# Performance work log

Hardware: AMD Instinct MI355X
Metric: run time of the kernel (lower is better)

Reference implementation:

```python
import jax, jax.numpy as jnp
import numpy as np

B, N, C = 8, 1024, 768
H, D = 12, 64  # num_heads, head_dim
SCALE = D ** -0.5


def setup_inputs() -> dict:
    key = jax.random.key(0)
    ks = jax.random.split(key, 6)
    x = jax.random.normal(ks[0], (B, N, C), dtype=jnp.float32)
    # per-head Linear weights stacked: [H, D, C] (torch Linear stores [out, in])
    Wq = jax.random.normal(ks[1], (H, D, C), dtype=jnp.float32) * 0.02
    Wk = jax.random.normal(ks[2], (H, D, C), dtype=jnp.float32) * 0.02
    Wv = jax.random.normal(ks[3], (H, D, C), dtype=jnp.float32) * 0.02
    Wp = jax.random.normal(ks[4], (C, C), dtype=jnp.float32) * 0.02
    bp = jnp.zeros((C,), dtype=jnp.float32)
    return {"x": x, "Wq": Wq, "Wk": Wk, "Wv": Wv, "Wp": Wp, "bp": bp}


def reference(x, Wq, Wk, Wv, Wp, bp):
    # Per-head projections (batched across heads): [B, H, N, D]
    q = jnp.einsum('bnc,hdc->bhnd', x, Wq) * SCALE
    k = jnp.einsum('bnc,hdc->bhnd', x, Wk)
    v = jnp.einsum('bnc,hdc->bhnd', x, Wv)
    # Scaled dot-product attention per head
    attn = jax.nn.softmax(jnp.einsum('bhnd,bhmd->bhnm', q, k), axis=-1)
    out = jnp.einsum('bhnm,bhmd->bhnd', attn, v)
    # Concat heads along last dim == transpose to [B, N, H, D] then reshape
    out = out.transpose(0, 2, 1, 3).reshape(x.shape[0], x.shape[1], -1)
    # Output projection
    return out @ Wp.T + bp
```

## Files before the change

kernel.cpp:

```cpp
#include <hip/hip_runtime.h>

typedef unsigned short u16;
typedef __attribute__((ext_vector_type(8))) __bf16 bf16x8;
typedef __attribute__((ext_vector_type(4))) float f32x4;
typedef __attribute__((ext_vector_type(16))) float f32x16;

__device__ __forceinline__ u16 f2bf(float f) {
    union { float f; unsigned u; } v; v.f = f;
    unsigned u = v.u;
    u += 0x7FFFu + ((u >> 16) & 1u);
    return (u16)(u >> 16);
}

__device__ __forceinline__ unsigned pk2(float lo, float hi) {
    union { __bf16 h[2]; unsigned u; } x;
    x.h[0] = (__bf16)lo; x.h[1] = (__bf16)hi;
    return x.u;
}
__device__ __forceinline__ void pswap(unsigned &a, unsigned &b) {
    auto r = __builtin_amdgcn_permlane32_swap(a, b, false, false);
    a = r[0]; b = r[1];
}

typedef const __attribute__((address_space(1))) void GV;
typedef __attribute__((address_space(3))) void LV;
__device__ __forceinline__ void gl2lds16(const void* g, void* l) {
    __builtin_amdgcn_global_load_lds((GV*)g, (LV*)l, 16, 0, 0);
}

__global__ __launch_bounds__(256) void cast_all(
    const float* __restrict__ x,  const float* __restrict__ Wq,
    const float* __restrict__ Wk, const float* __restrict__ Wv,
    const float* __restrict__ Wp,
    u16* __restrict__ xb, u16* __restrict__ wb, u16* __restrict__ wpb)
{
    int bid = blockIdx.x;
    const float4* s; ushort4* d; int idx;
    if (bid < 6144) {
        s = (const float4*)x; d = (ushort4*)xb; idx = bid * 256 + threadIdx.x;
    } else {
        int t = bid - 6144;
        int w = t / 576;
        idx = (t - w * 576) * 256 + threadIdx.x;
        s = (const float4*)(w == 0 ? Wq : w == 1 ? Wk : w == 2 ? Wv : Wp);
        d = (ushort4*)(w == 3 ? wpb : wb + w * 589824);
    }
    float4 f = s[idx];
    ushort4 o;
    o.x = f2bf(f.x); o.y = f2bf(f.y); o.z = f2bf(f.z); o.w = f2bf(f.w);
    d[idx] = o;
}

__device__ __forceinline__ void stage_g(const u16* src, int k0, u16* lds, int g, int tid) {
    int i = g * 512 + tid;
    int row = i >> 3, p = i & 7;
    int l = p ^ (row & 7);
    gl2lds16(src + (size_t)row * 768 + k0 + l * 8, lds + i * 8);
}
__device__ __forceinline__ const bf16x8* frag64(const u16* lds, int row, int kc) {
    return reinterpret_cast<const bf16x8*>(lds + row * 64 + ((kc ^ (row & 7)) * 8));
}

__device__ __forceinline__ void kloop256(
    const u16* __restrict__ aSrc, const u16* __restrict__ bSrc,
    u16* As, u16* Bs, f32x4 (&acc)[4][4],
    int tid, int wm, int wn, int quad, int l16)
{
    #pragma unroll
    for (int tt = 0; tt < 2; tt++) {
        #pragma unroll
        for (int g = 0; g < 4; g++) stage_g(aSrc, tt * 64, As + tt * 16384, g, tid);
        #pragma unroll
        for (int g = 0; g < 2; g++) stage_g(bSrc, tt * 64, Bs + tt * 8192, g, tid);
    }
    asm volatile("s_waitcnt vmcnt(6)" ::: "memory");
    __builtin_amdgcn_s_barrier();
    asm volatile("" ::: "memory");

    int buf = 0;
    for (int t = 0; t < 12; t++) {
        const u16* Ab = As + buf * 16384;
        const u16* Bb = Bs + buf * 8192;
        int sb = buf + 2; if (sb >= 3) sb -= 3;
        u16* Asb = As + sb * 16384;
        u16* Bsb = Bs + sb * 8192;
        const bool pf = (t + 2 < 12);
        const int k2 = (t + 2) * 64;

        bf16x8 a[4], b[4];
        #pragma unroll
        for (int mi = 0; mi < 4; mi++) a[mi] = *frag64(Ab, wm * 64 + mi * 16 + l16, quad);
        #pragma unroll
        for (int ni = 0; ni < 4; ni++) b[ni] = *frag64(Bb, wn * 64 + ni * 16 + l16, quad);
        if (pf) {
            stage_g(aSrc, k2, Asb, 0, tid);
            stage_g(aSrc, k2, Asb, 1, tid);
            stage_g(aSrc, k2, Asb, 2, tid);
        }
        __builtin_amdgcn_s_barrier();
        asm volatile("" ::: "memory");
        __builtin_amdgcn_s_setprio(1);
        #pragma unroll
        for (int mi = 0; mi < 4; mi++)
            #pragma unroll
            for (int ni = 0; ni < 4; ni++)
                acc[mi][ni] = __builtin_amdgcn_mfma_f32_16x16x32_bf16(a[mi], b[ni], acc[mi][ni], 0, 0, 0);
        __builtin_amdgcn_s_setprio(0);

        #pragma unroll
        for (int mi = 0; mi < 4; mi++) a[mi] = *frag64(Ab, wm * 64 + mi * 16 + l16, 4 + quad);
        #pragma unroll
        for (int ni = 0; ni < 4; ni++) b[ni] = *frag64(Bb, wn * 64 + ni * 16 + l16, 4 + quad);
        if (pf) {
            stage_g(aSrc, k2, Asb, 3, tid);
            stage_g(bSrc, k2, Bsb, 0, tid);
            stage_g(bSrc, k2, Bsb, 1, tid);
        }
        if (t <= 9)       asm volatile("s_waitcnt vmcnt(6)" ::: "memory");
        else if (t == 10) asm volatile("s_waitcnt vmcnt(0)" ::: "memory");
        __builtin_amdgcn_s_barrier();
        asm volatile("" ::: "memory");
        __builtin_amdgcn_s_setprio(1);
        #pragma unroll
        for (int mi = 0; mi < 4; mi++)
            #pragma unroll
            for (int ni = 0; ni < 4; ni++)
                acc[mi][ni] = __builtin_amdgcn_mfma_f32_16x16x32_bf16(a[mi], b[ni], acc[mi][ni], 0, 0, 0);
        __builtin_amdgcn_s_setprio(0);

        buf++; if (buf == 3) buf = 0;
    }
}

__global__ __launch_bounds__(512, 2) void gemm_qkv(
    const u16* __restrict__ A, const u16* __restrict__ Bm,
    u16* __restrict__ qo, u16* __restrict__ ko, u16* __restrict__ vto)
{
    __shared__ u16 As[3][16384];
    __shared__ u16 Bs[3][8192];
    const int tid = threadIdx.x;
    const int wave = tid >> 6, lane = tid & 63;
    const int quad = lane >> 4, l16 = lane & 15;
    const int wm = wave >> 1, wn = wave & 1;
    const int id = blockIdx.x + 18 * blockIdx.y;
    const int nid = (id & 7) * 72 + (id >> 3);
    const int bx = nid % 18, by = nid / 18;
    const int rowBase = by * 256;
    const int colBase = bx * 128;

    f32x4 acc[4][4] = {};
    kloop256(A + (size_t)rowBase * 768, Bm + (size_t)colBase * 768,
             &As[0][0], &Bs[0][0], acc, tid, wm, wn, quad, l16);

    #pragma unroll
    for (int mi = 0; mi < 4; mi++) {
        #pragma unroll
        for (int ni = 0; ni < 4; ni++) {
            int gj = colBase + wn * 64 + ni * 16 + l16;
            int which = gj / 768;
            int r = gj - which * 768;
            int h = r >> 6, d = r & 63;
            int gi0 = rowBase + wm * 64 + mi * 16 + quad * 4;
            int b_ = gi0 >> 10;
            int n0 = gi0 & 1023;
            if (which == 2) {
                ushort4 pk;
                pk.x = f2bf(acc[mi][ni][0]);
                pk.y = f2bf(acc[mi][ni][1]);
                pk.z = f2bf(acc[mi][ni][2]);
                pk.w = f2bf(acc[mi][ni][3]);
                *reinterpret_cast<ushort4*>(vto + ((size_t)(b_ * 12 + h) * 64 + d) * 1024 + n0) = pk;
            } else {
                float s = (which == 0) ? 0.125f : 1.0f;
                u16* dst = (which == 0 ? qo : ko) + ((size_t)(b_ * 12 + h) * 1024 + n0) * 64 + d;
                #pragma unroll
                for (int rr = 0; rr < 4; rr++)
                    dst[(size_t)rr * 64] = f2bf(acc[mi][ni][rr] * s);
            }
        }
    }
}

__global__ __launch_bounds__(256, 3) void attn_fwd(
    const u16* __restrict__ q, const u16* __restrict__ k,
    const u16* __restrict__ vt, u16* __restrict__ ao)
{
    __shared__ u16 Ks[2][4096];
    __shared__ u16 Vs[2][4096];
    const int bh = blockIdx.x, qt = blockIdx.y;
    const int b = bh / 12, h = bh - b * 12;
    const int tid = threadIdx.x;
    const int wave = tid >> 6, lane = tid & 63;
    const int l31 = lane & 31, hi = lane >> 5;
    const int sw = l31 & 7;

    const u16* qb = q + (size_t)bh * 65536 + ((size_t)qt * 128 + wave * 32) * 64;
    const u16* kb = k + (size_t)bh * 65536;
    const u16* vb = vt + (size_t)bh * 65536;

    auto stage = [&](int buf, int j0) {
        #pragma unroll
        for (int r = 0; r < 2; r++) {
            int i = r * 256 + tid;
            int row = i >> 3, cp = i & 7;
            int cl = cp ^ (row & 7);
            gl2lds16((const char*)kb + (size_t)(j0 + row) * 128 + cl * 16,
                     (char*)&Ks[buf][0] + i * 16);
        }
        #pragma unroll
        for (int r = 0; r < 2; r++) {
            int i = r * 256 + tid;
            int row = i >> 3, cp = i & 7;
            int cl = cp ^ (row & 7);
            gl2lds16((const char*)vb + (size_t)row * 2048 + (size_t)j0 * 2 + cl * 16,
                     (char*)&Vs[buf][0] + i * 16);
        }
    };

    stage(0, 0);

    bf16x8 qf[4];
    #pragma unroll
    for (int dk = 0; dk < 4; dk++)
        qf[dk] = *reinterpret_cast<const bf16x8*>(qb + l31 * 64 + dk * 16 + hi * 8);

    f32x16 o0 = {}, o1 = {};
    float lsum = 0.f;

    __syncthreads();

    int buf = 0;
    for (int j0 = 0; j0 < 1024; j0 += 64) {
        if (j0 + 64 < 1024) stage(buf ^ 1, j0 + 64);

        f32x16 s0 = {}, s1 = {};
        #pragma unroll
        for (int dk = 0; dk < 4; dk++) {
            int ch = ((2 * dk + hi) ^ sw) * 8;
            bf16x8 kf0 = *reinterpret_cast<const bf16x8*>(&Ks[buf][l31 * 64 + ch]);
            bf16x8 kf1 = *reinterpret_cast<const bf16x8*>(&Ks[buf][(32 + l31) * 64 + ch]);
            s0 = __builtin_amdgcn_mfma_f32_32x32x16_bf16(kf0, qf[dk], s0, 0, 0, 0);
            s1 = __builtin_amdgcn_mfma_f32_32x32x16_bf16(kf1, qf[dk], s1, 0, 0, 0);
        }

        bf16x8 pa[4];
        #pragma unroll
        for (int kbk = 0; kbk < 2; kbk++) {
            float p[16];
            #pragma unroll
            for (int r = 0; r < 16; r++) {
                p[r] = __expf(kbk ? s1[r] : s0[r]);
                lsum += p[r];
            }
            unsigned W00 = pk2(p[0],  p[1]),  W01 = pk2(p[2],  p[3]);
            unsigned W10 = pk2(p[4],  p[5]),  W11 = pk2(p[6],  p[7]);
            unsigned W20 = pk2(p[8],  p[9]),  W21 = pk2(p[10], p[11]);
            unsigned W30 = pk2(p[12], p[13]), W31 = pk2(p[14], p[15]);
            pswap(W00, W10); pswap(W01, W11);
            pswap(W20, W30); pswap(W21, W31);
            union { unsigned u[4]; bf16x8 v; } pk0, pk1;
            pk0.u[0] = W00; pk0.u[1] = W01; pk0.u[2] = W10; pk0.u[3] = W11;
            pk1.u[0] = W20; pk1.u[1] = W21; pk1.u[2] = W30; pk1.u[3] = W31;
            pa[kbk * 2 + 0] = pk0.v;
            pa[kbk * 2 + 1] = pk1.v;
        }

        #pragma unroll
        for (int ks = 0; ks < 4; ks++) {
            int ch = ((2 * ks + hi) ^ sw) * 8;
            bf16x8 vf0 = *reinterpret_cast<const bf16x8*>(&Vs[buf][l31 * 64 + ch]);
            bf16x8 vf1 = *reinterpret_cast<const bf16x8*>(&Vs[buf][(32 + l31) * 64 + ch]);
            o0 = __builtin_amdgcn_mfma_f32_32x32x16_bf16(pa[ks], vf0, o0, 0, 0, 0);
            o1 = __builtin_amdgcn_mfma_f32_32x32x16_bf16(pa[ks], vf1, o1, 0, 0, 0);
        }

        __syncthreads();
        buf ^= 1;
    }

    lsum += __shfl_xor(lsum, 32, 64);

    #pragma unroll
    for (int r = 0; r < 16; r++) {
        int qrow = (r & 3) + 8 * (r >> 2) + 4 * hi;
        float lv = __shfl(lsum, qrow, 32);
        float inv = 1.0f / lv;
        int n = qt * 128 + wave * 32 + qrow;
        size_t base = (size_t)(b * 1024 + n) * 768 + h * 64;
        ao[base + l31]      = f2bf(o0[r] * inv);
        ao[base + 32 + l31] = f2bf(o1[r] * inv);
    }
}

__global__ __launch_bounds__(512, 2) void gemm_proj(
    const u16* __restrict__ A, const u16* __restrict__ Bm,
    const float* __restrict__ bias, float* __restrict__ out)
{
    __shared__ u16 As[3][16384];
    __shared__ u16 Bs[3][8192];
    const int tid = threadIdx.x;
    const int wave = tid >> 6, lane = tid & 63;
    const int quad = lane >> 4, l16 = lane & 15;
    const int wm = wave >> 1, wn = wave & 1;
    const int id = blockIdx.x + 6 * blockIdx.y;
    const int nid = (id & 7) * 24 + (id >> 3);
    const int bx = nid % 6, by = nid / 6;
    const int rowBase = by * 256;
    const int colBase = bx * 128;

    f32x4 acc[4][4] = {};
    kloop256(A + (size_t)rowBase * 768, Bm + (size_t)colBase * 768,
             &As[0][0], &Bs[0][0], acc, tid, wm, wn, quad, l16);

    #pragma unroll
    for (int mi = 0; mi < 4; mi++) {
        #pragma unroll
        for (int ni = 0; ni < 4; ni++) {
            int gj = colBase + wn * 64 + ni * 16 + l16;
            float bv = bias[gj];
            int gi0 = rowBase + wm * 64 + mi * 16 + quad * 4;
            #pragma unroll
            for (int rr2 = 0; rr2 < 4; rr2++)
                out[(size_t)(gi0 + rr2) * 768 + gj] = acc[mi][ni][rr2] + bv;
        }
    }
}

extern "C" void kernel_launch(void* const* d_in, const int* in_sizes, int n_in,
                              void* d_out, int out_size, void* d_ws, size_t ws_size,
                              hipStream_t stream) {
    const float* x  = (const float*)d_in[0];
    const float* Wq = (const float*)d_in[1];
    const float* Wk = (const float*)d_in[2];
    const float* Wv = (const float*)d_in[3];
    const float* Wp = (const float*)d_in[4];
    const float* bp = (const float*)d_in[5];
    float* out = (float*)d_out;

    u16* xb  = (u16*)d_ws;
    u16* wb  = xb  + 6291456;
    u16* wpb = wb  + 1769472;
    u16* qo  = wpb + 589824;
    u16* ko  = qo  + 6291456;
    u16* vto = ko  + 6291456;
    u16* ao  = vto + 6291456;

    cast_all<<<8448, 256, 0, stream>>>(x, Wq, Wk, Wv, Wp, xb, wb, wpb);
    gemm_qkv<<<dim3(18, 32), 512, 0, stream>>>(xb, wb, qo, ko, vto);
    attn_fwd<<<dim3(96, 8), 256, 0, stream>>>(qo, ko, vto, ao);
    gemm_proj<<<dim3(6, 32), 512, 0, stream>>>(ao, wpb, bp, out);
}
```

Measured before the change: 189.4 us.

## Halve GEMM K-step to 32 with new LDS layout and smaller proj tiles

Both GEMMs now step K by 32 instead of 64 and use a new swizzled LDS layout that packs two rows per 64-element line. This shrinks shared memory per block so more blocks fit per CU (the launch bounds ask for 4 blocks for qkv and 3 for proj). The projection GEMM is retiled to 128x128 blocks of 256 threads, which doubles its grid to raise occupancy and fill the GPU better. The cost is twice as many loop iterations and barriers, with less MFMA work between each synchronisation.

Measured after the change: 187.3 us. Within noise of the previous version (-1.1%).

```diff
diff --git a/kernel.cpp b/kernel.cpp
--- a/kernel.cpp
+++ b/kernel.cpp
@@ -51,93 +51,24 @@
     d[idx] = o;
 }
 
-__device__ __forceinline__ void stage_g(const u16* src, int k0, u16* lds, int g, int tid) {
-    int i = g * 512 + tid;
-    int row = i >> 3, p = i & 7;
-    int l = p ^ (row & 7);
-    gl2lds16(src + (size_t)row * 768 + k0 + l * 8, lds + i * 8);
-}
-__device__ __forceinline__ const bf16x8* frag64(const u16* lds, int row, int kc) {
-    return reinterpret_cast<const bf16x8*>(lds + row * 64 + ((kc ^ (row & 7)) * 8));
-}
-
-__device__ __forceinline__ void kloop256(
-    const u16* __restrict__ aSrc, const u16* __restrict__ bSrc,
-    u16* As, u16* Bs, f32x4 (&acc)[4][4],
-    int tid, int wm, int wn, int quad, int l16)
-{
-    #pragma unroll
-    for (int tt = 0; tt < 2; tt++) {
-        #pragma unroll
-        for (int g = 0; g < 4; g++) stage_g(aSrc, tt * 64, As + tt * 16384, g, tid);
-        #pragma unroll
-        for (int g = 0; g < 2; g++) stage_g(bSrc, tt * 64, Bs + tt * 8192, g, tid);
-    }
-    asm volatile("s_waitcnt vmcnt(6)" ::: "memory");
-    __builtin_amdgcn_s_barrier();
-    asm volatile("" ::: "memory");
-
-    int buf = 0;
-    for (int t = 0; t < 12; t++) {
-        const u16* Ab = As + buf * 16384;
-        const u16* Bb = Bs + buf * 8192;
-        int sb = buf + 2; if (sb >= 3) sb -= 3;
-        u16* Asb = As + sb * 16384;
-        u16* Bsb = Bs + sb * 8192;
-        const bool pf = (t + 2 < 12);
-        const int k2 = (t + 2) * 64;
-
-        bf16x8 a[4], b[4];
-        #pragma unroll
-        for (int mi = 0; mi < 4; mi++) a[mi] = *frag64(Ab, wm * 64 + mi * 16 + l16, quad);
-        #pragma unroll
-        for (int ni = 0; ni < 4; ni++) b[ni] = *frag64(Bb, wn * 64 + ni * 16 + l16, quad);
-        if (pf) {
-            stage_g(aSrc, k2, Asb, 0, tid);
-            stage_g(aSrc, k2, Asb, 1, tid);
-            stage_g(aSrc, k2, Asb, 2, tid);
-        }
-        __builtin_amdgcn_s_barrier();
-        asm volatile("" ::: "memory");
-        __builtin_amdgcn_s_setprio(1);
-        #pragma unroll
-        for (int mi = 0; mi < 4; mi++)
-            #pragma unroll
-            for (int ni = 0; ni < 4; ni++)
-                acc[mi][ni] = __builtin_amdgcn_mfma_f32_16x16x32_bf16(a[mi], b[ni], acc[mi][ni], 0, 0, 0);
-        __builtin_amdgcn_s_setprio(0);
-
-        #pragma unroll
-        for (int mi = 0; mi < 4; mi++) a[mi] = *frag64(Ab, wm * 64 + mi * 16 + l16, 4 + quad);
-        #pragma unroll
-        for (int ni = 0; ni < 4; ni++) b[ni] = *frag64(Bb, wn * 64 + ni * 16 + l16, 4 + quad);
-        if (pf) {
-            stage_g(aSrc, k2, Asb, 3, tid);
-            stage_g(bSrc, k2, Bsb, 0, tid);
-            stage_g(bSrc, k2, Bsb, 1, tid);
-        }
-        if (t <= 9)       asm volatile("s_waitcnt vmcnt(6)" ::: "memory");
-        else if (t == 10) asm volatile("s_waitcnt vmcnt(0)" ::: "memory");
-        __builtin_amdgcn_s_barrier();
-        asm volatile("" ::: "memory");
-        __builtin_amdgcn_s_setprio(1);
-        #pragma unroll
-        for (int mi = 0; mi < 4; mi++)
-            #pragma unroll
-            for (int ni = 0; ni < 4; ni++)
-                acc[mi][ni] = __builtin_amdgcn_mfma_f32_16x16x32_bf16(a[mi], b[ni], acc[mi][ni], 0, 0, 0);
-        __builtin_amdgcn_s_setprio(0);
-
-        buf++; if (buf == 3) buf = 0;
-    }
-}
-
-__global__ __launch_bounds__(512, 2) void gemm_qkv(
+__device__ __forceinline__ void stage_c(const u16* src, int k0, u16* lds, int i) {
+    int line = i >> 3, pos = i & 7;
+    int p = pos ^ (line & 7);
+    int r = line * 2 + (p >> 2), c = p & 3;
+    gl2lds16(src + (size_t)r * 768 + k0 + c * 8, lds + i * 8);
+}
+__device__ __forceinline__ const bf16x8* fragK(const u16* lds, int row, int quad) {
+    int line = row >> 1;
+    int pos = (((row & 1) << 2) | quad) ^ (line & 7);
+    return reinterpret_cast<const bf16x8*>(lds + line * 64 + pos * 8);
+}
+
+__global__ __launch_bounds__(512, 4) void gemm_qkv(
     const u16* __restrict__ A, const u16* __restrict__ Bm,
     u16* __restrict__ qo, u16* __restrict__ ko, u16* __restrict__ vto)
 {
-    __shared__ u16 As[3][16384];
-    __shared__ u16 Bs[3][8192];
+    __shared__ u16 As[3][8192];
+    __shared__ u16 Bs[3][4096];
     const int tid = threadIdx.x;
     const int wave = tid >> 6, lane = tid & 63;
     const int quad = lane >> 4, l16 = lane & 15;
@@ -148,9 +79,47 @@
     const int rowBase = by * 256;
     const int colBase = bx * 128;
 
+    const u16* aSrc = A + (size_t)rowBase * 768;
+    const u16* bSrc = Bm + (size_t)colBase * 768;
     f32x4 acc[4][4] = {};
-    kloop256(A + (size_t)rowBase * 768, Bm + (size_t)colBase * 768,
-             &As[0][0], &Bs[0][0], acc, tid, wm, wn, quad, l16);
+
+    #pragma unroll
+    for (int tt = 0; tt < 2; tt++) {
+        stage_c(aSrc, tt * 32, As[tt], tid);
+        stage_c(aSrc, tt * 32, As[tt], 512 + tid);
+        stage_c(bSrc, tt * 32, Bs[tt], tid);
+    }
+    asm volatile("s_waitcnt vmcnt(3)" ::: "memory");
+    __builtin_amdgcn_s_barrier();
+    asm volatile("" ::: "memory");
+
+    int buf = 0;
+    for (int t = 0; t < 24; t++) {
+        bf16x8 a[4], b[4];
+        #pragma unroll
+        for (int mi = 0; mi < 4; mi++) a[mi] = *fragK(As[buf], wm * 64 + mi * 16 + l16, quad);
+        #pragma unroll
+        for (int ni = 0; ni < 4; ni++) b[ni] = *fragK(Bs[buf], wn * 64 + ni * 16 + l16, quad);
+        int sb = buf + 2; if (sb >= 3) sb -= 3;
+        if (t + 2 < 24) {
+            int k2 = (t + 2) * 32;
+            stage_c(aSrc, k2, As[sb], tid);
+            stage_c(aSrc, k2, As[sb], 512 + tid);
+            stage_c(bSrc, k2, Bs[sb], tid);
+        }
+        if (t <= 21)      asm volatile("s_waitcnt vmcnt(3)" ::: "memory");
+        else if (t == 22) asm volatile("s_waitcnt vmcnt(0)" ::: "memory");
+        __builtin_amdgcn_s_barrier();
+        asm volatile("" ::: "memory");
+        __builtin_amdgcn_s_setprio(1);
+        #pragma unroll
+        for (int mi = 0; mi < 4; mi++)
+            #pragma unroll
+            for (int ni = 0; ni < 4; ni++)
+                acc[mi][ni] = __builtin_amdgcn_mfma_f32_16x16x32_bf16(a[mi], b[ni], acc[mi][ni], 0, 0, 0);
+        __builtin_amdgcn_s_setprio(0);
+        buf = (buf == 2) ? 0 : buf + 1;
+    }
 
     #pragma unroll
     for (int mi = 0; mi < 4; mi++) {
@@ -292,33 +261,73 @@
     }
 }
 
-__global__ __launch_bounds__(512, 2) void gemm_proj(
+__global__ __launch_bounds__(256, 3) void gemm_proj(
     const u16* __restrict__ A, const u16* __restrict__ Bm,
     const float* __restrict__ bias, float* __restrict__ out)
 {
-    __shared__ u16 As[3][16384];
-    __shared__ u16 Bs[3][8192];
+    __shared__ u16 As[3][4096];
+    __shared__ u16 Bs[3][4096];
     const int tid = threadIdx.x;
     const int wave = tid >> 6, lane = tid & 63;
     const int quad = lane >> 4, l16 = lane & 15;
-    const int wm = wave >> 1, wn = wave & 1;
+    const int wr = (wave >> 1) * 64, wc = (wave & 1) * 64;
     const int id = blockIdx.x + 6 * blockIdx.y;
-    const int nid = (id & 7) * 24 + (id >> 3);
+    const int nid = (id & 7) * 48 + (id >> 3);
     const int bx = nid % 6, by = nid / 6;
-    const int rowBase = by * 256;
+    const int rowBase = by * 128;
     const int colBase = bx * 128;
 
+    const u16* aSrc = A + (size_t)rowBase * 768;
+    const u16* bSrc = Bm + (size_t)colBase * 768;
     f32x4 acc[4][4] = {};
-    kloop256(A + (size_t)rowBase * 768, Bm + (size_t)colBase * 768,
-             &As[0][0], &Bs[0][0], acc, tid, wm, wn, quad, l16);
+
+    #pragma unroll
+    for (int tt = 0; tt < 2; tt++) {
+        stage_c(aSrc, tt * 32, As[tt], tid);
+        stage_c(aSrc, tt * 32, As[tt], 256 + tid);
+        stage_c(bSrc, tt * 32, Bs[tt], tid);
+        stage_c(bSrc, tt * 32, Bs[tt], 256 + tid);
+    }
+    asm volatile("s_waitcnt vmcnt(4)" ::: "memory");
+    __builtin_amdgcn_s_barrier();
+    asm volatile("" ::: "memory");
+
+    int buf = 0;
+    for (int t = 0; t < 24; t++) {
+        bf16x8 a[4], b[4];
+        #pragma unroll
+        for (int mi = 0; mi < 4; mi++) a[mi] = *fragK(As[buf], wr + mi * 16 + l16, quad);
+        #pragma unroll
+        for (int ni = 0; ni < 4; ni++) b[ni] = *fragK(Bs[buf], wc + ni * 16 + l16, quad);
+        int sb = buf + 2; if (sb >= 3) sb -= 3;
+        if (t + 2 < 24) {
+            int k2 = (t + 2) * 32;
+            stage_c(aSrc, k2, As[sb], tid);
+            stage_c(aSrc, k2, As[sb], 256 + tid);
+            stage_c(bSrc, k2, Bs[sb], tid);
+            stage_c(bSrc, k2, Bs[sb], 256 + tid);
+        }
+        if (t <= 21)      asm volatile("s_waitcnt vmcnt(4)" ::: "memory");
+        else if (t == 22) asm volatile("s_waitcnt vmcnt(0)" ::: "memory");
+        __builtin_amdgcn_s_barrier();
+        asm volatile("" ::: "memory");
+        __builtin_amdgcn_s_setprio(1);
+        #pragma unroll
+        for (int mi = 0; mi < 4; mi++)
+            #pragma unroll
+            for (int ni = 0; ni < 4; ni++)
+                acc[mi][ni] = __builtin_amdgcn_mfma_f32_16x16x32_bf16(a[mi], b[ni], acc[mi][ni], 0, 0, 0);
+        __builtin_amdgcn_s_setprio(0);
+        buf = (buf == 2) ? 0 : buf + 1;
+    }
 
     #pragma unroll
     for (int mi = 0; mi < 4; mi++) {
         #pragma unroll
         for (int ni = 0; ni < 4; ni++) {
-            int gj = colBase + wn * 64 + ni * 16 + l16;
+            int gj = colBase + wc + ni * 16 + l16;
             float bv = bias[gj];
-            int gi0 = rowBase + wm * 64 + mi * 16 + quad * 4;
+            int gi0 = rowBase + wr + mi * 16 + quad * 4;
             #pragma unroll
             for (int rr2 = 0; rr2 < 4; rr2++)
                 out[(size_t)(gi0 + rr2) * 768 + gj] = acc[mi][ni][rr2] + bv;
@@ -348,5 +357,5 @@
     cast_all<<<8448, 256, 0, stream>>>(x, Wq, Wk, Wv, Wp, xb, wb, wpb);
     gemm_qkv<<<dim3(18, 32), 512, 0, stream>>>(xb, wb, qo, ko, vto);
     attn_fwd<<<dim3(96, 8), 256, 0, stream>>>(qo, ko, vto, ao);
-    gemm_proj<<<dim3(6, 32), 512, 0, stream>>>(ao, wpb, bp, out);
-}
+    gemm_proj<<<dim3(6, 64), 256, 0, stream>>>(ao, wpb, bp, out);
+}
```
